# Kernel tuning notes

Measured on AMD Instinct MI355X. Metric: run time of the kernel, lower is better.

## Reference

```python
import jax, jax.numpy as jnp
import numpy as np

D, NH, NL, NP, DFF = 256, 8, 4, 4, 1024
HD = D // NH
SHAPES = np.array([[64, 64], [32, 32], [16, 16], [8, 8]], dtype=np.int32)  # (H, W) per level


def _layer_norm(x, g, b, eps=1e-5):
    mu = jnp.mean(x, -1, keepdims=True)
    var = jnp.mean((x - mu) ** 2, -1, keepdims=True)
    return (x - mu) * jax.lax.rsqrt(var + eps) * g + b


def _bilinear_sample(value_l, loc):
    # value_l: (N, H, W, NH, HD); loc: (N, Lq, NH, NP, 2) normalized to [0,1]
    # Matches F.grid_sample(align_corners=False, padding_mode='zeros') on grid 2*loc-1.
    N, H, W = value_l.shape[0], value_l.shape[1], value_l.shape[2]
    x = loc[..., 0] * W - 0.5
    y = loc[..., 1] * H - 0.5
    x0 = jnp.floor(x)
    y0 = jnp.floor(y)
    wx1 = x - x0
    wy1 = y - y0
    b_idx = jnp.arange(N)[:, None, None, None]
    h_idx = jnp.arange(NH)[None, None, :, None]

    def gather(yi, xi):
        valid = (yi >= 0) & (yi < H) & (xi >= 0) & (xi < W)
        yc = jnp.clip(yi, 0, H - 1).astype(jnp.int32)
        xc = jnp.clip(xi, 0, W - 1).astype(jnp.int32)
        v = value_l[b_idx, yc, xc, h_idx]  # (N, Lq, NH, NP, HD)
        return v * valid[..., None].astype(value_l.dtype)

    v00 = gather(y0, x0)
    v01 = gather(y0, x0 + 1)
    v10 = gather(y0 + 1, x0)
    v11 = gather(y0 + 1, x0 + 1)
    wx1 = wx1[..., None]
    wy1 = wy1[..., None]
    top = v00 * (1 - wx1) + v01 * wx1
    bot = v10 * (1 - wx1) + v11 * wx1
    return top * (1 - wy1) + bot * wy1  # (N, Lq, NH, NP, HD)


def setup_inputs() -> dict:
    key = jax.random.key(0)
    ks = jax.random.split(key, 24)
    N, Lq = 8, int(SHAPES.prod(axis=1).sum())  # 5440
    s = 0.02
    return {
        "src": jax.random.normal(ks[0], (N, Lq, D), jnp.float32),
        "pos": jax.random.normal(ks[1], (N, Lq, D), jnp.float32),
        "reference_points": jax.random.uniform(ks[2], (N, Lq, NL, 2), jnp.float32),
        "spatial_shapes": jnp.asarray(SHAPES),
        "W_value": s * jax.random.normal(ks[3], (D, D)),
        "b_value": jnp.zeros((D,)),
        "W_off": s * jax.random.normal(ks[4], (D, NH * NL * NP * 2)),
        "b_off": 0.5 * jax.random.normal(ks[5], (NH * NL * NP * 2,)),
        "W_attn": s * jax.random.normal(ks[6], (D, NH * NL * NP)),
        "b_attn": jnp.zeros((NH * NL * NP,)),
        "W_out": s * jax.random.normal(ks[7], (D, D)),
        "b_out": jnp.zeros((D,)),
        "ln1_g": jnp.ones((D,)),
        "ln1_b": jnp.zeros((D,)),
        "W1": s * jax.random.normal(ks[8], (D, DFF)),
        "b1": jnp.zeros((DFF,)),
        "W2": s * jax.random.normal(ks[9], (DFF, D)),
        "b2": jnp.zeros((D,)),
        "ln2_g": jnp.ones((D,)),
        "ln2_b": jnp.zeros((D,)),
    }


def reference(src, pos, reference_points, spatial_shapes,
              W_value, b_value, W_off, b_off, W_attn, b_attn, W_out, b_out,
              ln1_g, ln1_b, W1, b1, W2, b2, ln2_g, ln2_b):
    shapes = np.asarray(spatial_shapes)  # static (NL, 2)
    N, Lq = src.shape[0], src.shape[1]

    # --- MSDeformAttn ---
    query = src + pos
    value = (src @ W_value + b_value).reshape(N, Lq, NH, HD)
    offsets = (query @ W_off + b_off).reshape(N, Lq, NH, NL, NP, 2)
    attn = jax.nn.softmax((query @ W_attn + b_attn).reshape(N, Lq, NH, NL * NP), axis=-1)
    attn = attn.reshape(N, Lq, NH, NL, NP)
    # offset normalizer is (W, H) per level
    norm = jnp.asarray(np.stack([shapes[:, 1], shapes[:, 0]], -1), jnp.float32)  # (NL, 2)
    loc = reference_points[:, :, None, :, None, :] + offsets / norm[None, None, None, :, None, :]

    out = jnp.zeros((N, Lq, NH, HD), src.dtype)
    start = 0
    for l in range(NL):
        H, W = int(shapes[l, 0]), int(shapes[l, 1])
        v_l = jax.lax.dynamic_slice_in_dim(value, start, H * W, axis=1).reshape(N, H, W, NH, HD)
        sampled = _bilinear_sample(v_l, loc[:, :, :, l])  # (N, Lq, NH, NP, HD)
        out = out + jnp.einsum('nqhp,nqhpd->nqhd', attn[:, :, :, l], sampled)
        start += H * W
    src2 = out.reshape(N, Lq, D) @ W_out + b_out

    # --- residual + norm + FFN (dropout=0, eval) ---
    x = _layer_norm(src + src2, ln1_g, ln1_b)
    ffn = jax.nn.relu(x @ W1 + b1) @ W2 + b2
    return _layer_norm(x + ffn, ln2_g, ln2_b)
```

## Files before the change

kernel.cpp:

```cpp
#include <hip/hip_runtime.h>
#include <math.h>

#define LQ_ 5440
#define NB_ 8
#define NQ_ (NB_ * LQ_)
#define D_  256
#define NH_ 8
#define HD_ 32

typedef __attribute__((ext_vector_type(8))) short short8;
typedef __attribute__((ext_vector_type(4))) float f32x4;

__device__ __forceinline__ ushort f2bf(float f) {
    union { float f; unsigned u; } v; v.f = f;
    unsigned u = v.u;
    unsigned r = (u + 0x7FFFu + ((u >> 16) & 1u)) >> 16;
    return (ushort)r;
}
__device__ __forceinline__ float bf2f(ushort u) {
    union { unsigned u; float f; } v; v.u = ((unsigned)u) << 16; return v.f;
}

__device__ __forceinline__ void gload_lds16(const void* g, void* l) {
    __builtin_amdgcn_global_load_lds(
        (const __attribute__((address_space(1))) void*)g,
        (__attribute__((address_space(3))) void*)l, 16, 0, 0);
}

__device__ __forceinline__ void wg_barrier() {
    __builtin_amdgcn_sched_barrier(0);
    __builtin_amdgcn_s_barrier();
    __builtin_amdgcn_sched_barrier(0);
}

#define TPREP_ 736

__global__ __launch_bounds__(256)
void prep(const float* __restrict__ src, const float* __restrict__ pos,
          ushort* __restrict__ s_bf, ushort* __restrict__ q_bf,
          const float* __restrict__ Wv, const float* __restrict__ Woff,
          const float* __restrict__ Wattn, const float* __restrict__ Wout,
          const float* __restrict__ W1, const float* __restrict__ W2,
          ushort* __restrict__ Wv_t, ushort* __restrict__ Woff_t,
          ushort* __restrict__ Wattn_t, ushort* __restrict__ Wout_t,
          ushort* __restrict__ W1_t, ushort* __restrict__ W2_t) {
    __shared__ float tile[32][33];
    const int bid = blockIdx.x;
    const int tid = threadIdx.x;

    if (bid >= TPREP_) {
        const int i = (bid - TPREP_) * 256 + tid;
        const float4 s = ((const float4*)src)[i];
        const float4 p = ((const float4*)pos)[i];
        ushort4 a, b;
        a.x = f2bf(s.x); a.y = f2bf(s.y); a.z = f2bf(s.z); a.w = f2bf(s.w);
        b.x = f2bf(s.x + p.x); b.y = f2bf(s.y + p.y);
        b.z = f2bf(s.z + p.z); b.w = f2bf(s.w + p.w);
        ((ushort4*)s_bf)[i] = a;
        ((ushort4*)q_bf)[i] = b;
        return;
    }

    const float* W; ushort* Wt; int K, N, bx, by;
    if (bid < 64)       { W = Wv;    Wt = Wv_t;    K = 256;  N = 256;  bx = bid % 8;         by = bid / 8; }
    else if (bid < 128) { W = Woff;  Wt = Woff_t;  K = 256;  N = 256;  bx = (bid-64) % 8;    by = (bid-64) / 8; }
    else if (bid < 160) { W = Wattn; Wt = Wattn_t; K = 256;  N = 128;  bx = (bid-128) % 4;   by = (bid-128) / 4; }
    else if (bid < 224) { W = Wout;  Wt = Wout_t;  K = 256;  N = 256;  bx = (bid-160) % 8;   by = (bid-160) / 8; }
    else if (bid < 480) { W = W1;    Wt = W1_t;    K = 256;  N = 1024; bx = (bid-224) % 32;  by = (bid-224) / 32; }
    else                { W = W2;    Wt = W2_t;    K = 1024; N = 256;  bx = (bid-480) % 8;   by = (bid-480) / 8; }

    const int tx = tid & 31;
    const int ty = tid >> 5;
    for (int i = ty; i < 32; i += 8)
        tile[i][tx] = W[(size_t)(by * 32 + i) * N + bx * 32 + tx];
    __syncthreads();
    for (int i = ty; i < 32; i += 8)
        Wt[(size_t)(bx * 32 + i) * K + by * 32 + tx] = f2bf(tile[tx][i]);
}

#define BM 128
#define BN 128
#define BK 64

__device__ __forceinline__ void gemm_body(
    ushort* __restrict__ lAb, ushort* __restrict__ lBb,
    const ushort* __restrict__ A, const ushort* __restrict__ Bt,
    const float* __restrict__ bias, float* __restrict__ Cf,
    ushort* __restrict__ Cb, int N, int K, int relu, int col0, int row0) {
    const int t    = threadIdx.x;
    const int w    = t >> 6;
    const int lr   = t & 15;
    const int quad = (t >> 4) & 3;
    const int wm   = (w >> 1) * 64;
    const int wn   = (w & 1) * 64;

    f32x4 acc[4][4];
    #pragma unroll
    for (int i = 0; i < 4; ++i)
        #pragma unroll
        for (int j = 0; j < 4; ++j)
            acc[i][j] = (f32x4){0.f, 0.f, 0.f, 0.f};

    const int sr = t >> 3;
    const int sc = (t & 7) * 8;
    const size_t aoff = (size_t)(row0 + sr) * K + sc;
    const size_t boff = (size_t)(col0 + sr) * K + sc;
    const int wb = w * 1024;

    auto stage = [&](int buf, int k0) {
        char* la = (char*)(lAb + buf * (BM * BK)) + wb;
        char* lb = (char*)(lBb + buf * (BN * BK)) + wb;
        #pragma unroll
        for (int g = 0; g < 4; ++g) {
            gload_lds16(A  + aoff + k0 + (size_t)g * 32 * K, la + g * 4096);
            gload_lds16(Bt + boff + k0 + (size_t)g * 32 * K, lb + g * 4096);
        }
    };

    stage(0, 0);
    int cur = 0;
    for (int k0 = 0; k0 < K; k0 += BK) {
        if (k0 + BK < K) {
            stage(cur ^ 1, k0 + BK);
            asm volatile("s_waitcnt vmcnt(8)" ::: "memory");
        } else {
            asm volatile("s_waitcnt vmcnt(0)" ::: "memory");
        }
        wg_barrier();
        const ushort* pA = lAb + cur * (BM * BK);
        const ushort* pB = lBb + cur * (BN * BK);
        #pragma unroll
        for (int kk = 0; kk < 2; ++kk) {
            short8 af[4], bfr[4];
            #pragma unroll
            for (int i = 0; i < 4; ++i)
                af[i] = *(const short8*)(pA + (wm + i * 16 + lr) * BK + kk * 32 + quad * 8);
            #pragma unroll
            for (int j = 0; j < 4; ++j)
                bfr[j] = *(const short8*)(pB + (wn + j * 16 + lr) * BK + kk * 32 + quad * 8);
            #pragma unroll
            for (int i = 0; i < 4; ++i)
                #pragma unroll
                for (int j = 0; j < 4; ++j)
                    acc[i][j] = __builtin_amdgcn_mfma_f32_16x16x32_bf16(af[i], bfr[j], acc[i][j], 0, 0, 0);
        }
        wg_barrier();
        cur ^= 1;
    }

    #pragma unroll
    for (int j = 0; j < 4; ++j) {
        const int col = col0 + wn + j * 16 + lr;
        const float bb = bias ? bias[col] : 0.f;
        #pragma unroll
        for (int i = 0; i < 4; ++i) {
            const int rbase = row0 + wm + i * 16 + quad * 4;
            #pragma unroll
            for (int r = 0; r < 4; ++r) {
                float v = acc[i][j][r] + bb;
                if (relu) v = fmaxf(v, 0.f);
                if (Cf) Cf[(size_t)(rbase + r) * N + col] = v;
                else    Cb[(size_t)(rbase + r) * N + col] = f2bf(v);
            }
        }
    }
}

__global__ __launch_bounds__(256)
void mfma_gemm(const ushort* __restrict__ A, const ushort* __restrict__ Bt,
               const float* __restrict__ bias, float* __restrict__ Cf,
               ushort* __restrict__ Cb, int N, int K, int relu) {
    __shared__ ushort lA[2][BM * BK];
    __shared__ ushort lB[2][BN * BK];
    const int nt   = gridDim.x;
    const int nwg  = nt * gridDim.y;
    const int flat = blockIdx.y * nt + blockIdx.x;
    const int xc   = flat & 7;
    const int sl   = flat >> 3;
    const int q8   = nwg >> 3;
    const int rm8  = nwg & 7;
    const int wi   = (xc < rm8 ? xc * (q8 + 1) : rm8 * (q8 + 1) + (xc - rm8) * q8) + sl;
    gemm_body(&lA[0][0], &lB[0][0], A, Bt, bias, Cf, Cb, N, K, relu,
              (wi % nt) * BN, (wi / nt) * BM);
}

__global__ __launch_bounds__(256)
void gemm_vc(const ushort* __restrict__ s_bf, const ushort* __restrict__ q_bf,
             const ushort* __restrict__ Wv_t, const ushort* __restrict__ Woff_t,
             const float* __restrict__ b_value,
             ushort* __restrict__ val_bf, ushort* __restrict__ comb_bf) {
    __shared__ ushort lA[2][BM * BK];
    __shared__ ushort lB[2][BN * BK];
    const int nwg  = gridDim.x;
    const int flat = blockIdx.x;
    const int xc   = flat & 7;
    const int sl   = flat >> 3;
    const int q8   = nwg >> 3;
    const int rm8  = nwg & 7;
    const int wi   = (xc < rm8 ? xc * (q8 + 1) : rm8 * (q8 + 1) + (xc - rm8) * q8) + sl;
    const int ci   = wi % 5;
    const int row0 = (wi / 5) * BM;
    if (ci < 2)
        gemm_body(&lA[0][0], &lB[0][0], s_bf, Wv_t, b_value, nullptr, val_bf,
                  256, 256, 0, ci * BN, row0);
    else
        gemm_body(&lA[0][0], &lB[0][0], q_bf, Woff_t, nullptr, nullptr, comb_bf,
                  384, 256, 0, (ci - 2) * BN, row0);
}

__global__ __launch_bounds__(256)
void msda_sample(const ushort* __restrict__ value, const ushort* __restrict__ comb,
                 const float* __restrict__ b_off, const float* __restrict__ b_attn,
                 const float* __restrict__ refp, ushort* __restrict__ out) {
    __shared__ int   s_addr[256][4];
    __shared__ float s_w[256][4];

    const int t   = threadIdx.x;
    const int tq  = t >> 7;
    const int u   = t & 127;
    const int bid = blockIdx.x;
    const int swz = (bid & 7) * (NQ_ / 2 / 8) + (bid >> 3);
    const int nq  = swz * 2 + tq;
    const int n   = nq / LQ_;

    {
        const int h = u >> 4;
        const int p = u & 15;
        const int l = p >> 2;

        const int starts[4] = {0, 4096, 5120, 5376};
        const int Wl = 64 >> l;

        float a = bf2f(comb[(size_t)nq * 384 + 256 + u]) + b_attn[u];
        float m = a;
        #pragma unroll
        for (int o = 8; o > 0; o >>= 1) m = fmaxf(m, __shfl_xor(m, o));
        float e = __expf(a - m);
        float s = e;
        #pragma unroll
        for (int o = 8; o > 0; o >>= 1) s += __shfl_xor(s, o);
        const float wgt = e / s;

        const float rx = refp[(size_t)nq * 8 + l * 2 + 0];
        const float ry = refp[(size_t)nq * 8 + l * 2 + 1];
        const uint  opk = *(const uint*)(comb + (size_t)nq * 384 + u * 2);
        const float ox = bf2f((ushort)(opk & 0xffffu))  + b_off[u * 2 + 0];
        const float oy = bf2f((ushort)(opk >> 16))      + b_off[u * 2 + 1];

        const float fw = (float)Wl;
        const float x  = (rx + ox / fw) * fw - 0.5f;
        const float y  = (ry + oy / fw) * fw - 0.5f;
        const float x0f = floorf(x), y0f = floorf(y);
        const int   x0 = (int)x0f, y0 = (int)y0f;
        const float wx1 = x - x0f, wy1 = y - y0f;
        const float wx0 = 1.f - wx1, wy0 = 1.f - wy1;

        const float xm0 = (x0 >= 0 && x0 < Wl) ? 1.f : 0.f;
        const float xm1 = (x0 + 1 >= 0 && x0 + 1 < Wl) ? 1.f : 0.f;
        const float ym0 = (y0 >= 0 && y0 < Wl) ? 1.f : 0.f;
        const float ym1 = (y0 + 1 >= 0 && y0 + 1 < Wl) ? 1.f : 0.f;

        const int x0c = min(max(x0, 0), Wl - 1);
        const int x1c = min(max(x0 + 1, 0), Wl - 1);
        const int y0c = min(max(y0, 0), Wl - 1);
        const int y1c = min(max(y0 + 1, 0), Wl - 1);

        const int base = (n * LQ_ + starts[l]) * 512 + h * 64;
        s_addr[t][0] = base + (y0c * Wl + x0c) * 512;
        s_addr[t][1] = base + (y0c * Wl + x1c) * 512;
        s_addr[t][2] = base + (y1c * Wl + x0c) * 512;
        s_addr[t][3] = base + (y1c * Wl + x1c) * 512;
        s_w[t][0] = wgt * wy0 * wx0 * ym0 * xm0;
        s_w[t][1] = wgt * wy0 * wx1 * ym0 * xm1;
        s_w[t][2] = wgt * wy1 * wx0 * ym1 * xm0;
        s_w[t][3] = wgt * wy1 * wx1 * ym1 * xm1;
    }
    __syncthreads();

    {
        const int h   = u >> 4;
        const int d2  = u & 15;
        const int sb  = tq * 128 + h * 16;
        const uint dby = (uint)(d2 * 4);
        const char* vbase = (const char*)value;

        float acc0 = 0.f, acc1 = 0.f;
        #pragma unroll 8
        for (int p = 0; p < 16; ++p) {
            const int*   ap = s_addr[sb + p];
            const float* wp = s_w[sb + p];
            #pragma unroll
            for (int c = 0; c < 4; ++c) {
                const uint v = *(const uint*)(vbase + ((uint)ap[c] + dby));
                const float w = wp[c];
                union { uint u; float f; } lo, hi;
                lo.u = v << 16;
                hi.u = v & 0xffff0000u;
                acc0 = fmaf(lo.f, w, acc0);
                acc1 = fmaf(hi.f, w, acc1);
            }
        }
        const uint packed = (uint)f2bf(acc0) | ((uint)f2bf(acc1) << 16);
        ((uint*)out)[(size_t)nq * 128 + u] = packed;
    }
}

__global__ __launch_bounds__(256)
void add_ln(const float* __restrict__ a, const float* __restrict__ b,
            const float* __restrict__ g, const float* __restrict__ be,
            float* __restrict__ xf, ushort* __restrict__ xb) {
    const int row  = blockIdx.x * 4 + (threadIdx.x >> 6);
    const int lane = threadIdx.x & 63;
    const size_t base = (size_t)row * 256 + lane * 4;

    const float4 av = *(const float4*)(a + base);
    const float4 bv = *(const float4*)(b + base);
    float4 x;
    x.x = av.x + bv.x; x.y = av.y + bv.y; x.z = av.z + bv.z; x.w = av.w + bv.w;

    float s = x.x + x.y + x.z + x.w;
    #pragma unroll
    for (int o = 32; o > 0; o >>= 1) s += __shfl_xor(s, o);
    const float mu = s * (1.f / 256.f);

    float4 dx;
    dx.x = x.x - mu; dx.y = x.y - mu; dx.z = x.z - mu; dx.w = x.w - mu;
    float vv = dx.x * dx.x + dx.y * dx.y + dx.z * dx.z + dx.w * dx.w;
    #pragma unroll
    for (int o = 32; o > 0; o >>= 1) vv += __shfl_xor(vv, o);
    const float rstd = rsqrtf(vv * (1.f / 256.f) + 1e-5f);

    const float4 gv  = *(const float4*)(g  + lane * 4);
    const float4 bev = *(const float4*)(be + lane * 4);
    float4 y;
    y.x = dx.x * rstd * gv.x + bev.x;
    y.y = dx.y * rstd * gv.y + bev.y;
    y.z = dx.z * rstd * gv.z + bev.z;
    y.w = dx.w * rstd * gv.w + bev.w;

    *(float4*)(xf + base) = y;
    if (xb) {
        ushort4 yb;
        yb.x = f2bf(y.x); yb.y = f2bf(y.y); yb.z = f2bf(y.z); yb.w = f2bf(y.w);
        *(ushort4*)(xb + base) = yb;
    }
}

extern "C" void kernel_launch(void* const* d_in, const int* in_sizes, int n_in,
                              void* d_out, int out_size, void* d_ws, size_t ws_size,
                              hipStream_t stream) {
    const float* src     = (const float*)d_in[0];
    const float* pos     = (const float*)d_in[1];
    const float* refp    = (const float*)d_in[2];
    const float* W_value = (const float*)d_in[4];
    const float* b_value = (const float*)d_in[5];
    const float* W_off   = (const float*)d_in[6];
    const float* b_off   = (const float*)d_in[7];
    const float* W_attn  = (const float*)d_in[8];
    const float* b_attn  = (const float*)d_in[9];
    const float* W_out   = (const float*)d_in[10];
    const float* b_out   = (const float*)d_in[11];
    const float* ln1g    = (const float*)d_in[12];
    const float* ln1b    = (const float*)d_in[13];
    const float* W1      = (const float*)d_in[14];
    const float* b1      = (const float*)d_in[15];
    const float* W2      = (const float*)d_in[16];
    const float* b2      = (const float*)d_in[17];
    const float* ln2g    = (const float*)d_in[18];
    const float* ln2b    = (const float*)d_in[19];
    float* out = (float*)d_out;
    char*  ws  = (char*)d_ws;

    const size_t SZ_BF  = (size_t)NQ_ * 256 * 2;
    const size_t SZ_CB  = (size_t)NQ_ * 384 * 2;
    const size_t SZ_F   = (size_t)NQ_ * 256 * 4;
    ushort* s_bf    = (ushort*)(ws);
    ushort* q_bf    = (ushort*)(ws + SZ_BF);
    ushort* val_bf  = (ushort*)(ws + 2 * SZ_BF);
    ushort* comb    = (ushort*)(ws + 3 * SZ_BF);
    ushort* samp_bf = (ushort*)(ws + 3 * SZ_BF + SZ_CB);
    ushort* h_bf    = (ushort*)(ws);
    ushort* x_bf    = (ushort*)(ws + 3 * SZ_BF + SZ_CB);
    char*   wbase   = ws + 3 * SZ_BF + SZ_CB + SZ_BF;
    ushort* Wv_t    = (ushort*)(wbase);
    ushort* Woff_t  = (ushort*)(wbase + 131072);
    ushort* Wattn_t = (ushort*)(wbase + 262144);
    ushort* Wout_t  = (ushort*)(wbase + 327680);
    ushort* W1_t    = (ushort*)(wbase + 458752);
    ushort* W2_t    = (ushort*)(wbase + 983040);
    char*   fbase   = wbase + 1507328;
    float*  src2    = (float*)(fbase);
    float*  xf      = (float*)(fbase + SZ_F);

    prep<<<dim3(TPREP_ + (NQ_ * 256 / 4) / 256), 256, 0, stream>>>(
        src, pos, s_bf, q_bf, W_value, W_off, W_attn, W_out, W1, W2,
        Wv_t, Woff_t, Wattn_t, Wout_t, W1_t, W2_t);

    const int MT = NQ_ / BM;

    gemm_vc<<<dim3(5 * MT), 256, 0, stream>>>(s_bf, q_bf, Wv_t, Woff_t, b_value, val_bf, comb);
    msda_sample<<<dim3(NQ_ / 2), 256, 0, stream>>>(val_bf, comb, b_off, b_attn, refp, samp_bf);
    mfma_gemm<<<dim3(2, MT), 256, 0, stream>>>(samp_bf, Wout_t, b_out, src2, nullptr, 256, 256, 0);
    add_ln<<<dim3(NQ_ / 4), 256, 0, stream>>>(src, src2, ln1g, ln1b, xf, x_bf);
    mfma_gemm<<<dim3(8, MT), 256, 0, stream>>>(x_bf, W1_t, b1, nullptr, h_bf, 1024, 256, 1);
    mfma_gemm<<<dim3(2, MT), 256, 0, stream>>>(h_bf, W2_t, b2, src2, nullptr, 256, 1024, 0);
    add_ln<<<dim3(NQ_ / 4), 256, 0, stream>>>(xf, src2, ln2g, ln2b, out, nullptr);
}
```

Before: 440.0 us.

## Fuse output and FFN2 GEMMs with residual add and LayerNorm

Adds a gemm_ln kernel that computes a 64x256 full-row tile, adds bias and residual, and performs LayerNorm in the epilogue using a cross-wave LDS reduction. It replaces the two GEMM+add_ln pairs, removing the fp32 src2 intermediate round trip and two kernel launches. The tile covers the full N=256 width, so each block loads the whole B matrix and the grid shrinks to 680 blocks. Variance is computed as E[x^2]-mu^2, which is less numerically stable than the previous two-pass form.

```diff
diff --git a/kernel.cpp b/kernel.cpp
--- a/kernel.cpp
+++ b/kernel.cpp
@@ -31,6 +31,14 @@
     __builtin_amdgcn_sched_barrier(0);
     __builtin_amdgcn_s_barrier();
     __builtin_amdgcn_sched_barrier(0);
+}
+
+__device__ __forceinline__ int xcd_swz(int flat, int nwg) {
+    const int xc  = flat & 7;
+    const int sl  = flat >> 3;
+    const int q8  = nwg >> 3;
+    const int rm8 = nwg & 7;
+    return (xc < rm8 ? xc * (q8 + 1) : rm8 * (q8 + 1) + (xc - rm8) * q8) + sl;
 }
 
 #define TPREP_ 736
@@ -172,14 +180,8 @@
                ushort* __restrict__ Cb, int N, int K, int relu) {
     __shared__ ushort lA[2][BM * BK];
     __shared__ ushort lB[2][BN * BK];
-    const int nt   = gridDim.x;
-    const int nwg  = nt * gridDim.y;
-    const int flat = blockIdx.y * nt + blockIdx.x;
-    const int xc   = flat & 7;
-    const int sl   = flat >> 3;
-    const int q8   = nwg >> 3;
-    const int rm8  = nwg & 7;
-    const int wi   = (xc < rm8 ? xc * (q8 + 1) : rm8 * (q8 + 1) + (xc - rm8) * q8) + sl;
+    const int nt  = gridDim.x;
+    const int wi  = xcd_swz(blockIdx.y * nt + blockIdx.x, nt * gridDim.y);
     gemm_body(&lA[0][0], &lB[0][0], A, Bt, bias, Cf, Cb, N, K, relu,
               (wi % nt) * BN, (wi / nt) * BM);
 }
@@ -191,13 +193,7 @@
              ushort* __restrict__ val_bf, ushort* __restrict__ comb_bf) {
     __shared__ ushort lA[2][BM * BK];
     __shared__ ushort lB[2][BN * BK];
-    const int nwg  = gridDim.x;
-    const int flat = blockIdx.x;
-    const int xc   = flat & 7;
-    const int sl   = flat >> 3;
-    const int q8   = nwg >> 3;
-    const int rm8  = nwg & 7;
-    const int wi   = (xc < rm8 ? xc * (q8 + 1) : rm8 * (q8 + 1) + (xc - rm8) * q8) + sl;
+    const int wi   = xcd_swz(blockIdx.x, gridDim.x);
     const int ci   = wi % 5;
     const int row0 = (wi / 5) * BM;
     if (ci < 2)
@@ -208,6 +204,144 @@
                   384, 256, 0, (ci - 2) * BN, row0);
 }
 
+#define GM 64
+#define GN 256
+
+__global__ __launch_bounds__(256)
+void gemm_ln(const ushort* __restrict__ A, const ushort* __restrict__ Bt,
+             const float* __restrict__ bias, const float* __restrict__ res,
+             float* __restrict__ outf, ushort* __restrict__ outb,
+             const float* __restrict__ g, const float* __restrict__ be, int K) {
+    __shared__ ushort lA[2][GM * BK];
+    __shared__ ushort lB[2][GN * BK];
+    const int t    = threadIdx.x;
+    const int wi   = xcd_swz(blockIdx.x, gridDim.x);
+    const int row0 = wi * GM;
+    const int w    = t >> 6;
+    const int lr   = t & 15;
+    const int quad = (t >> 4) & 3;
+    const int wn   = w * 64;
+
+    f32x4 acc[4][4];
+    #pragma unroll
+    for (int i = 0; i < 4; ++i)
+        #pragma unroll
+        for (int j = 0; j < 4; ++j)
+            acc[i][j] = (f32x4){0.f, 0.f, 0.f, 0.f};
+
+    const int sr = t >> 3;
+    const int sc = (t & 7) * 8;
+    const size_t aoff = (size_t)(row0 + sr) * K + sc;
+    const size_t boff = (size_t)sr * K + sc;
+    const int wb = w * 1024;
+
+    auto stage = [&](int buf, int k0) {
+        char* la = (char*)(lA[buf]) + wb;
+        char* lb = (char*)(lB[buf]) + wb;
+        #pragma unroll
+        for (int ga = 0; ga < 2; ++ga)
+            gload_lds16(A + aoff + k0 + (size_t)ga * 32 * K, la + ga * 4096);
+        #pragma unroll
+        for (int gb = 0; gb < 8; ++gb)
+            gload_lds16(Bt + boff + k0 + (size_t)gb * 32 * K, lb + gb * 4096);
+    };
+
+    stage(0, 0);
+    int cur = 0;
+    for (int k0 = 0; k0 < K; k0 += BK) {
+        if (k0 + BK < K) {
+            stage(cur ^ 1, k0 + BK);
+            asm volatile("s_waitcnt vmcnt(10)" ::: "memory");
+        } else {
+            asm volatile("s_waitcnt vmcnt(0)" ::: "memory");
+        }
+        wg_barrier();
+        const ushort* pA = lA[cur];
+        const ushort* pB = lB[cur];
+        #pragma unroll
+        for (int kk = 0; kk < 2; ++kk) {
+            short8 af[4], bfr[4];
+            #pragma unroll
+            for (int i = 0; i < 4; ++i)
+                af[i] = *(const short8*)(pA + (i * 16 + lr) * BK + kk * 32 + quad * 8);
+            #pragma unroll
+            for (int j = 0; j < 4; ++j)
+                bfr[j] = *(const short8*)(pB + (wn + j * 16 + lr) * BK + kk * 32 + quad * 8);
+            #pragma unroll
+            for (int i = 0; i < 4; ++i)
+                #pragma unroll
+                for (int j = 0; j < 4; ++j)
+                    acc[i][j] = __builtin_amdgcn_mfma_f32_16x16x32_bf16(af[i], bfr[j], acc[i][j], 0, 0, 0);
+        }
+        wg_barrier();
+        cur ^= 1;
+    }
+
+    #pragma unroll
+    for (int j = 0; j < 4; ++j) {
+        const int col = wn + j * 16 + lr;
+        const float bb = bias[col];
+        #pragma unroll
+        for (int i = 0; i < 4; ++i) {
+            const int rbase = row0 + i * 16 + quad * 4;
+            #pragma unroll
+            for (int r = 0; r < 4; ++r)
+                acc[i][j][r] += bb + res[(size_t)(rbase + r) * 256 + col];
+        }
+    }
+
+    float* reds = (float*)&lA[0][0];
+    float* redq = reds + 256;
+    float mu[4][4], rstd[4][4];
+    #pragma unroll
+    for (int i = 0; i < 4; ++i)
+        #pragma unroll
+        for (int r = 0; r < 4; ++r) {
+            float s = acc[i][0][r] + acc[i][1][r] + acc[i][2][r] + acc[i][3][r];
+            float q = acc[i][0][r]*acc[i][0][r] + acc[i][1][r]*acc[i][1][r]
+                    + acc[i][2][r]*acc[i][2][r] + acc[i][3][r]*acc[i][3][r];
+            #pragma unroll
+            for (int o = 1; o < 16; o <<= 1) {
+                s += __shfl_xor(s, o);
+                q += __shfl_xor(q, o);
+            }
+            if (lr == 0) {
+                const int rl = i * 16 + quad * 4 + r;
+                reds[w * 64 + rl] = s;
+                redq[w * 64 + rl] = q;
+            }
+        }
+    __syncthreads();
+    #pragma unroll
+    for (int i = 0; i < 4; ++i)
+        #pragma unroll
+        for (int r = 0; r < 4; ++r) {
+            const int rl = i * 16 + quad * 4 + r;
+            const float s = reds[rl] + reds[64 + rl] + reds[128 + rl] + reds[192 + rl];
+            const float q = redq[rl] + redq[64 + rl] + redq[128 + rl] + redq[192 + rl];
+            const float m = s * (1.f / 256.f);
+            mu[i][r]   = m;
+            rstd[i][r] = rsqrtf(q * (1.f / 256.f) - m * m + 1e-5f);
+        }
+
+    #pragma unroll
+    for (int j = 0; j < 4; ++j) {
+        const int col = wn + j * 16 + lr;
+        const float gc = g[col];
+        const float bc = be[col];
+        #pragma unroll
+        for (int i = 0; i < 4; ++i) {
+            const int rbase = row0 + i * 16 + quad * 4;
+            #pragma unroll
+            for (int r = 0; r < 4; ++r) {
+                const float y = (acc[i][j][r] - mu[i][r]) * rstd[i][r] * gc + bc;
+                if (outf) outf[(size_t)(rbase + r) * 256 + col] = y;
+                if (outb) outb[(size_t)(rbase + r) * 256 + col] = f2bf(y);
+            }
+        }
+    }
+}
+
 __global__ __launch_bounds__(256)
 void msda_sample(const ushort* __restrict__ value, const ushort* __restrict__ comb,
                  const float* __restrict__ b_off, const float* __restrict__ b_attn,
@@ -244,8 +378,8 @@
         const float rx = refp[(size_t)nq * 8 + l * 2 + 0];
         const float ry = refp[(size_t)nq * 8 + l * 2 + 1];
         const uint  opk = *(const uint*)(comb + (size_t)nq * 384 + u * 2);
-        const float ox = bf2f((ushort)(opk & 0xffffu))  + b_off[u * 2 + 0];
-        const float oy = bf2f((ushort)(opk >> 16))      + b_off[u * 2 + 1];
+        const float ox = bf2f((ushort)(opk & 0xffffu)) + b_off[u * 2 + 0];
+        const float oy = bf2f((ushort)(opk >> 16))     + b_off[u * 2 + 1];
 
         const float fw = (float)Wl;
         const float x  = (rx + ox / fw) * fw - 0.5f;
@@ -302,47 +436,6 @@
         }
         const uint packed = (uint)f2bf(acc0) | ((uint)f2bf(acc1) << 16);
         ((uint*)out)[(size_t)nq * 128 + u] = packed;
-    }
-}
-
-__global__ __launch_bounds__(256)
-void add_ln(const float* __restrict__ a, const float* __restrict__ b,
-            const float* __restrict__ g, const float* __restrict__ be,
-            float* __restrict__ xf, ushort* __restrict__ xb) {
-    const int row  = blockIdx.x * 4 + (threadIdx.x >> 6);
-    const int lane = threadIdx.x & 63;
-    const size_t base = (size_t)row * 256 + lane * 4;
-
-    const float4 av = *(const float4*)(a + base);
-    const float4 bv = *(const float4*)(b + base);
-    float4 x;
-    x.x = av.x + bv.x; x.y = av.y + bv.y; x.z = av.z + bv.z; x.w = av.w + bv.w;
-
-    float s = x.x + x.y + x.z + x.w;
-    #pragma unroll
-    for (int o = 32; o > 0; o >>= 1) s += __shfl_xor(s, o);
-    const float mu = s * (1.f / 256.f);
-
-    float4 dx;
-    dx.x = x.x - mu; dx.y = x.y - mu; dx.z = x.z - mu; dx.w = x.w - mu;
-    float vv = dx.x * dx.x + dx.y * dx.y + dx.z * dx.z + dx.w * dx.w;
-    #pragma unroll
-    for (int o = 32; o > 0; o >>= 1) vv += __shfl_xor(vv, o);
-    const float rstd = rsqrtf(vv * (1.f / 256.f) + 1e-5f);
-
-    const float4 gv  = *(const float4*)(g  + lane * 4);
-    const float4 bev = *(const float4*)(be + lane * 4);
-    float4 y;
-    y.x = dx.x * rstd * gv.x + bev.x;
-    y.y = dx.y * rstd * gv.y + bev.y;
-    y.z = dx.z * rstd * gv.z + bev.z;
-    y.w = dx.w * rstd * gv.w + bev.w;
-
-    *(float4*)(xf + base) = y;
-    if (xb) {
-        ushort4 yb;
-        yb.x = f2bf(y.x); yb.y = f2bf(y.y); yb.z = f2bf(y.z); yb.w = f2bf(y.w);
-        *(ushort4*)(xb + base) = yb;
     }
 }
 
@@ -380,7 +473,6 @@
     ushort* comb    = (ushort*)(ws + 3 * SZ_BF);
     ushort* samp_bf = (ushort*)(ws + 3 * SZ_BF + SZ_CB);
     ushort* h_bf    = (ushort*)(ws);
-    ushort* x_bf    = (ushort*)(ws + 3 * SZ_BF + SZ_CB);
     char*   wbase   = ws + 3 * SZ_BF + SZ_CB + SZ_BF;
     ushort* Wv_t    = (ushort*)(wbase);
     ushort* Woff_t  = (ushort*)(wbase + 131072);
@@ -389,8 +481,8 @@
     ushort* W1_t    = (ushort*)(wbase + 458752);
     ushort* W2_t    = (ushort*)(wbase + 983040);
     char*   fbase   = wbase + 1507328;
-    float*  src2    = (float*)(fbase);
-    float*  xf      = (float*)(fbase + SZ_F);
+    float*  xf      = (float*)(fbase);
+    ushort* x_bf    = (ushort*)(fbase + SZ_F);
 
     prep<<<dim3(TPREP_ + (NQ_ * 256 / 4) / 256), 256, 0, stream>>>(
         src, pos, s_bf, q_bf, W_value, W_off, W_attn, W_out, W1, W2,
@@ -400,9 +492,9 @@
 
     gemm_vc<<<dim3(5 * MT), 256, 0, stream>>>(s_bf, q_bf, Wv_t, Woff_t, b_value, val_bf, comb);
     msda_sample<<<dim3(NQ_ / 2), 256, 0, stream>>>(val_bf, comb, b_off, b_attn, refp, samp_bf);
-    mfma_gemm<<<dim3(2, MT), 256, 0, stream>>>(samp_bf, Wout_t, b_out, src2, nullptr, 256, 256, 0);
-    add_ln<<<dim3(NQ_ / 4), 256, 0, stream>>>(src, src2, ln1g, ln1b, xf, x_bf);
+    gemm_ln<<<dim3(NQ_ / GM), 256, 0, stream>>>(samp_bf, Wout_t, b_out, src,
+                                                xf, x_bf, ln1g, ln1b, 256);
     mfma_gemm<<<dim3(8, MT), 256, 0, stream>>>(x_bf, W1_t, b1, nullptr, h_bf, 1024, 256, 1);
-    mfma_gemm<<<dim3(2, MT), 256, 0, stream>>>(h_bf, W2_t, b2, src2, nullptr, 256, 1024, 0);
-    add_ln<<<dim3(NQ_ / 4), 256, 0, stream>>>(xf, src2, ln2g, ln2b, out, nullptr);
-}
+    gemm_ln<<<dim3(NQ_ / GM), 256, 0, stream>>>(h_bf, W2_t, b2, xf,
+                                                out, nullptr, ln2g, ln2b, 1024);
+}
```

New measurement: 465.0 us. 1.06x slower.
